# Kernel tuning notes

Hardware: AMD Instinct MI355X
Metric: run time of the kernel (lower is better)

## Reference

```python
import jax, jax.numpy as jnp
import numpy as np

N_NODES = 16  # superpixels per sample (gcn1 nodes)


def setup_inputs() -> dict:
    key = jax.random.key(0)
    ks = jax.random.split(key, 10)
    B, Cin, H, W = 32, 64, 112, 112
    Cout, H2, W2 = 128, 56, 56
    E = 64
    inp = {
        "B_for": jax.random.normal(ks[0], (B, Cin, H, W), jnp.float32),
        "B_fon": jax.random.normal(ks[1], (B, Cout, H2, W2), jnp.float32),
        "seg": jax.random.randint(ks[2], (B, H, W), 0, N_NODES, jnp.int32),
        "src": jax.random.randint(ks[3], (B, E), 0, N_NODES, jnp.int32),
        "dst": jax.random.randint(ks[4], (B, E), 0, N_NODES, jnp.int32),
        "conv_w": jax.random.normal(ks[5], (1, Cin), jnp.float32) * 0.1,
        "conv_b": jnp.zeros((1,), jnp.float32),
        "W1": jax.random.normal(ks[6], (4, 32), jnp.float32) * 0.3,
        "b1": jnp.zeros((32,), jnp.float32),
        "W2": jax.random.normal(ks[7], (32, Cout), jnp.float32) * 0.15,
        "b2": jnp.zeros((Cout,), jnp.float32),
        "fc_w": jax.random.normal(ks[8], (1, N_NODES), jnp.float32) * 0.2,
        "fc_b": jnp.zeros((1,), jnp.float32),
    }
    return inp


def _superpixel_features(L, seg):
    # L: [B,1,H,W] intensity; seg: [B,H,W] labels in [0, N_NODES)
    B, _, H, W = L.shape
    ids = (seg + jnp.arange(B, dtype=seg.dtype)[:, None, None] * N_NODES).reshape(-1)
    Lf = L[:, 0].reshape(-1)
    ones = jnp.ones_like(Lf)
    rows = jnp.broadcast_to(jnp.arange(H, dtype=L.dtype)[None, :, None], (B, H, W)).reshape(-1)
    cols = jnp.broadcast_to(jnp.arange(W, dtype=L.dtype)[None, None, :], (B, H, W)).reshape(-1)
    nseg = B * N_NODES
    cnt = jax.ops.segment_sum(ones, ids, num_segments=nseg)
    s_r = jax.ops.segment_sum(rows, ids, num_segments=nseg)
    s_c = jax.ops.segment_sum(cols, ids, num_segments=nseg)
    s_i = jax.ops.segment_sum(Lf, ids, num_segments=nseg)
    cnt_safe = jnp.maximum(cnt, 1.0)
    feats = jnp.stack([s_r / cnt_safe, s_c / cnt_safe, s_i / cnt_safe, cnt], axis=-1)
    feats = feats.reshape(B, N_NODES, 4)
    # normalize mean_intensity and area columns: (x - mean) / (std + 1), unbiased std
    sub = feats[..., 2:]
    mu = sub.mean(axis=1, keepdims=True)
    sd = jnp.std(sub, axis=1, keepdims=True, ddof=1)
    return jnp.concatenate([feats[..., :2], (sub - mu) / (sd + 1.0)], axis=-1)


def _graph_conv(A, nrm, X, Wt, bt):
    # DGL GraphConv, norm='both': D^{-1/2} A D^{-1/2} X W + b
    agg = jnp.einsum('bij,bjf->bif', A, nrm[..., None] * X)
    return nrm[..., None] * agg @ Wt + bt


def reference(B_for, B_fon, seg, src, dst, conv_w, conv_b, W1, b1, W2, b2, fc_w, fc_b):
    B = B_for.shape[0]
    # 1x1 conv -> single-channel intensity map L
    L = jnp.einsum('bchw,oc->bohw', B_for, conv_w) + conv_b[None, :, None, None]
    X = _superpixel_features(L, seg)  # [B, N, 4]
    # symmetric adjacency from edge list
    bidx = jnp.arange(B)[:, None]
    A = jnp.zeros((B, N_NODES, N_NODES), B_for.dtype)
    A = A.at[bidx, src, dst].set(1.0)
    A = A.at[bidx, dst, src].set(1.0)
    nrm = jnp.clip(A.sum(-1), 1.0, None) ** -0.5
    h1 = jax.nn.relu(_graph_conv(A, nrm, X, W1, b1))   # [B, N, 32]
    h2 = jax.nn.relu(_graph_conv(A, nrm, h1, W2, b2))  # [B, N, 128]
    # fc over nodes: Linear(N -> 1) applied to h2.T  => [B, 128]
    G = jnp.einsum('bnf,n->bf', h2, fc_w[0]) + fc_b[0]
    # broadcast-modulate dense CNN features
    return G[:, :, None, None] * B_fon
```

## Files before the change

### kernel.cpp

```cpp
#include <hip/hip_runtime.h>

#define NN 16
constexpr int BB = 32, CIN = 64, HH = 112, WW = 112;
constexpr int HWC = HH * WW;
constexpr int COUT = 128, HW2 = 56 * 56;
constexpr int NE = 64;
constexpr int NQ = HWC / 4;
constexpr int BPI = 13;
constexpr int PF4 = COUT * HW2 / 4;
constexpr int SBPB = 25;

__global__ __launch_bounds__(256) void k_conv_seg(
    const float* __restrict__ Bfor, const int* __restrict__ seg,
    const float* __restrict__ convw, float* __restrict__ part)
{
    __shared__ float w[CIN];
    __shared__ float acc[8 * 80];
    const int tid = threadIdx.x;
    const int b   = blockIdx.x / BPI;
    const int blk = blockIdx.x % BPI;

    if (tid < CIN) w[tid] = convw[tid];
    for (int i = tid; i < 8 * 80; i += 256) acc[i] = 0.f;
    __syncthreads();

    const int q = blk * 256 + tid;
    if (q < NQ) {
        const int p = q * 4;
        const float* base = Bfor + (size_t)b * CIN * HWC + p;

        float4 s = make_float4(0.f, 0.f, 0.f, 0.f);
        #pragma unroll
        for (int cb = 0; cb < 4; ++cb) {
            float4 v[16];
            #pragma unroll
            for (int j = 0; j < 16; ++j)
                v[j] = *reinterpret_cast<const float4*>(base + (size_t)(cb * 16 + j) * HWC);
            #pragma unroll
            for (int j = 0; j < 16; ++j) {
                const float wc = w[cb * 16 + j];
                s.x = fmaf(v[j].x, wc, s.x);
                s.y = fmaf(v[j].y, wc, s.y);
                s.z = fmaf(v[j].z, wc, s.z);
                s.w = fmaf(v[j].w, wc, s.w);
            }
        }

        const int4 sg = *reinterpret_cast<const int4*>(seg + (size_t)b * HWC + p);
        const float row  = (float)(p / WW);
        const float col0 = (float)(p % WW);
        const int k = tid & 7;
        float* a0 = &acc[k * 80];
        atomicAdd(a0 + sg.x * 5 + 0, row);
        atomicAdd(a0 + sg.x * 5 + 1, col0);
        atomicAdd(a0 + sg.x * 5 + 2, s.x);
        atomicAdd(a0 + sg.x * 5 + 3, 1.f);
        atomicAdd(a0 + sg.y * 5 + 0, row);
        atomicAdd(a0 + sg.y * 5 + 1, col0 + 1.f);
        atomicAdd(a0 + sg.y * 5 + 2, s.y);
        atomicAdd(a0 + sg.y * 5 + 3, 1.f);
        atomicAdd(a0 + sg.z * 5 + 0, row);
        atomicAdd(a0 + sg.z * 5 + 1, col0 + 2.f);
        atomicAdd(a0 + sg.z * 5 + 2, s.z);
        atomicAdd(a0 + sg.z * 5 + 3, 1.f);
        atomicAdd(a0 + sg.w * 5 + 0, row);
        atomicAdd(a0 + sg.w * 5 + 1, col0 + 3.f);
        atomicAdd(a0 + sg.w * 5 + 2, s.w);
        atomicAdd(a0 + sg.w * 5 + 3, 1.f);
    }
    __syncthreads();

    if (tid < NN * 4) {
        const int node = tid >> 2, st = tid & 3;
        float v = 0.f;
        #pragma unroll
        for (int k = 0; k < 8; ++k) v += acc[k * 80 + node * 5 + st];
        part[((b * BPI + blk) * NN + node) * 4 + st] = v;
    }
}

__global__ __launch_bounds__(256) void k_graph_scale(
    const float* __restrict__ part, const int* __restrict__ src,
    const int* __restrict__ dst,  const float* __restrict__ convb,
    const float* __restrict__ W1, const float* __restrict__ b1,
    const float* __restrict__ W2, const float* __restrict__ b2,
    const float* __restrict__ fcw, const float* __restrict__ fcb,
    const float* __restrict__ Bfon, float* __restrict__ out)
{
    const int b    = blockIdx.x / SBPB;
    const int blkb = blockIdx.x % SBPB;
    const int tid  = threadIdx.x;

    __shared__ float X[NN][4];
    __shared__ float A[NN][NN];
    __shared__ float nrm[NN];
    __shared__ float h1s[NN][32];
    __shared__ float agg[NN][32];
    __shared__ float gpart[2][COUT];
    __shared__ float Gs[COUT];

    if (tid < 64) {
        const int node = tid >> 2, st = tid & 3;
        float v = 0.f;
        #pragma unroll
        for (int k = 0; k < BPI; ++k) v += part[((b * BPI + k) * NN + node) * 4 + st];
        X[node][st] = v;
    }
    for (int i = tid; i < NN * NN; i += 256) ((float*)A)[i] = 0.f;
    __syncthreads();

    if (tid < NN) {
        const float cnt = X[tid][3];
        const float cs  = fmaxf(cnt, 1.f);
        X[tid][0] = X[tid][0] / cs;
        X[tid][1] = X[tid][1] / cs;
        X[tid][2] = (X[tid][2] + cnt * convb[0]) / cs;
    }
    __syncthreads();

    if (tid < 2) {
        const int c = 2 + tid;
        float mu = 0.f;
        for (int i = 0; i < NN; ++i) mu += X[i][c];
        mu *= (1.f / NN);
        float var = 0.f;
        for (int i = 0; i < NN; ++i) { const float d = X[i][c] - mu; var = fmaf(d, d, var); }
        var *= (1.f / (NN - 1));
        const float inv = 1.f / (sqrtf(var) + 1.f);
        for (int i = 0; i < NN; ++i) X[i][c] = (X[i][c] - mu) * inv;
    }
    if (tid >= 64 && tid < 64 + NE) {
        const int e = tid - 64;
        const int s = src[b * NE + e], d = dst[b * NE + e];
        A[s][d] = 1.f;
        A[d][s] = 1.f;
    }
    __syncthreads();

    if (tid < NN) {
        float rs = 0.f;
        for (int j = 0; j < NN; ++j) rs += A[tid][j];
        nrm[tid] = 1.f / sqrtf(fmaxf(rs, 1.f));
    }
    __syncthreads();

    if (tid < NN * 4) {
        const int i = tid >> 2, k = tid & 3;
        float s = 0.f;
        for (int j = 0; j < NN; ++j) s = fmaf(A[i][j] * nrm[j], X[j][k], s);
        agg[i][k] = s;
    }
    __syncthreads();

    for (int t = tid; t < NN * 32; t += 256) {
        const int i = t >> 5, f = t & 31;
        float s = 0.f;
        #pragma unroll
        for (int k = 0; k < 4; ++k) s = fmaf(agg[i][k], W1[k * 32 + f], s);
        h1s[i][f] = fmaxf(fmaf(nrm[i], s, b1[f]), 0.f);
    }
    __syncthreads();

    for (int t = tid; t < NN * 32; t += 256) {
        const int i = t >> 5, k = t & 31;
        float s = 0.f;
        for (int j = 0; j < NN; ++j) s = fmaf(A[i][j] * nrm[j], h1s[j][k], s);
        agg[i][k] = s;
    }
    __syncthreads();

    {
        const int f = tid & 127, half = tid >> 7;
        float g = 0.f;
        const float bf = b2[f];
        for (int i = half * 8; i < half * 8 + 8; ++i) {
            float s = 0.f;
            #pragma unroll
            for (int k = 0; k < 32; ++k) s = fmaf(agg[i][k], W2[k * COUT + f], s);
            g = fmaf(fcw[i], fmaxf(fmaf(nrm[i], s, bf), 0.f), g);
        }
        gpart[half][f] = g;
    }
    __syncthreads();
    if (tid < COUT) Gs[tid] = gpart[0][tid] + gpart[1][tid] + fcb[0];
    __syncthreads();

    const float4* bf4 = reinterpret_cast<const float4*>(Bfon) + (size_t)b * PF4;
    float4*       ob4 = reinterpret_cast<float4*>(out)        + (size_t)b * PF4;
    for (int t = blkb * 256 + tid; t < PF4; t += SBPB * 256) {
        const float4 v = bf4[t];
        const float  g = Gs[t / (HW2 / 4)];
        ob4[t] = make_float4(v.x * g, v.y * g, v.z * g, v.w * g);
    }
}

extern "C" void kernel_launch(void* const* d_in, const int* in_sizes, int n_in,
                              void* d_out, int out_size, void* d_ws, size_t ws_size,
                              hipStream_t stream)
{
    const float* Bfor  = (const float*)d_in[0];
    const float* Bfon  = (const float*)d_in[1];
    const int*   seg   = (const int*)d_in[2];
    const int*   src   = (const int*)d_in[3];
    const int*   dst   = (const int*)d_in[4];
    const float* convw = (const float*)d_in[5];
    const float* convb = (const float*)d_in[6];
    const float* W1    = (const float*)d_in[7];
    const float* b1    = (const float*)d_in[8];
    const float* W2    = (const float*)d_in[9];
    const float* b2    = (const float*)d_in[10];
    const float* fcw   = (const float*)d_in[11];
    const float* fcb   = (const float*)d_in[12];

    float* part = (float*)d_ws;
    float* out  = (float*)d_out;

    k_conv_seg<<<BB * BPI, 256, 0, stream>>>(Bfor, seg, convw, part);
    k_graph_scale<<<BB * SBPB, 256, 0, stream>>>(part, src, dst, convb,
                                                 W1, b1, W2, b2, fcw, fcb,
                                                 Bfon, out);
}
```

Baseline: 51.40 us.

## Split conv-seg work by channel group and image half per block

The first kernel now gives each block 8 input channels over half an image instead of all 64 channels over a 1024-pixel strip. Each thread keeps partial sums for 6-7 float4 pixel groups, and the row, column and count statistics are spread across channel groups 0-2. The graph kernel then sums 16 partials per sample. The aim is more independent loads in flight per block, at the cost of more seg reads and more shared-memory atomics for the intensity term (each channel group scatters its own partial).

```diff
diff --git a/kernel.cpp b/kernel.cpp
--- a/kernel.cpp
+++ b/kernel.cpp
@@ -6,76 +6,93 @@
 constexpr int COUT = 128, HW2 = 56 * 56;
 constexpr int NE = 64;
 constexpr int NQ = HWC / 4;
-constexpr int BPI = 13;
+constexpr int HQ = NQ / 2;
+constexpr int CPB = 8;
 constexpr int PF4 = COUT * HW2 / 4;
 constexpr int SBPB = 25;
 
-__global__ __launch_bounds__(256) void k_conv_seg(
+__global__ __launch_bounds__(256, 2) void k_conv_seg(
     const float* __restrict__ Bfor, const int* __restrict__ seg,
     const float* __restrict__ convw, float* __restrict__ part)
 {
-    __shared__ float w[CIN];
-    __shared__ float acc[8 * 80];
+    __shared__ float acc8[8 * 80];
     const int tid = threadIdx.x;
-    const int b   = blockIdx.x / BPI;
-    const int blk = blockIdx.x % BPI;
-
-    if (tid < CIN) w[tid] = convw[tid];
-    for (int i = tid; i < 8 * 80; i += 256) acc[i] = 0.f;
-    __syncthreads();
-
-    const int q = blk * 256 + tid;
-    if (q < NQ) {
-        const int p = q * 4;
-        const float* base = Bfor + (size_t)b * CIN * HWC + p;
-
-        float4 s = make_float4(0.f, 0.f, 0.f, 0.f);
-        #pragma unroll
-        for (int cb = 0; cb < 4; ++cb) {
-            float4 v[16];
-            #pragma unroll
-            for (int j = 0; j < 16; ++j)
-                v[j] = *reinterpret_cast<const float4*>(base + (size_t)(cb * 16 + j) * HWC);
-            #pragma unroll
-            for (int j = 0; j < 16; ++j) {
-                const float wc = w[cb * 16 + j];
-                s.x = fmaf(v[j].x, wc, s.x);
-                s.y = fmaf(v[j].y, wc, s.y);
-                s.z = fmaf(v[j].z, wc, s.z);
-                s.w = fmaf(v[j].w, wc, s.w);
-            }
-        }
-
-        const int4 sg = *reinterpret_cast<const int4*>(seg + (size_t)b * HWC + p);
-        const float row  = (float)(p / WW);
-        const float col0 = (float)(p % WW);
-        const int k = tid & 7;
-        float* a0 = &acc[k * 80];
-        atomicAdd(a0 + sg.x * 5 + 0, row);
-        atomicAdd(a0 + sg.x * 5 + 1, col0);
-        atomicAdd(a0 + sg.x * 5 + 2, s.x);
-        atomicAdd(a0 + sg.x * 5 + 3, 1.f);
-        atomicAdd(a0 + sg.y * 5 + 0, row);
-        atomicAdd(a0 + sg.y * 5 + 1, col0 + 1.f);
-        atomicAdd(a0 + sg.y * 5 + 2, s.y);
-        atomicAdd(a0 + sg.y * 5 + 3, 1.f);
-        atomicAdd(a0 + sg.z * 5 + 0, row);
-        atomicAdd(a0 + sg.z * 5 + 1, col0 + 2.f);
-        atomicAdd(a0 + sg.z * 5 + 2, s.z);
-        atomicAdd(a0 + sg.z * 5 + 3, 1.f);
-        atomicAdd(a0 + sg.w * 5 + 0, row);
-        atomicAdd(a0 + sg.w * 5 + 1, col0 + 3.f);
-        atomicAdd(a0 + sg.w * 5 + 2, s.w);
-        atomicAdd(a0 + sg.w * 5 + 3, 1.f);
-    }
-    __syncthreads();
-
-    if (tid < NN * 4) {
+    const int bid = blockIdx.x;
+    const int b   = bid >> 4;
+    const int h   = (bid >> 3) & 1;
+    const int cg  = bid & 7;
+
+    for (int i = tid; i < 8 * 80; i += 256) acc8[i] = 0.f;
+    __syncthreads();
+
+    float4 a[7];
+    #pragma unroll
+    for (int k = 0; k < 7; ++k) a[k] = make_float4(0.f, 0.f, 0.f, 0.f);
+
+    const float* bbase = Bfor + (size_t)(b * CIN + cg * CPB) * HWC + (size_t)h * HQ * 4;
+    #pragma unroll
+    for (int c = 0; c < CPB; ++c) {
+        const float wc = convw[cg * CPB + c];
+        const float* pl = bbase + (size_t)c * HWC + tid * 4;
+        float4 v[7];
+        #pragma unroll
+        for (int k = 0; k < 6; ++k)
+            v[k] = *reinterpret_cast<const float4*>(pl + k * 1024);
+        if (tid < 32) v[6] = *reinterpret_cast<const float4*>(pl + 6 * 1024);
+        #pragma unroll
+        for (int k = 0; k < 6; ++k) {
+            a[k].x = fmaf(v[k].x, wc, a[k].x);
+            a[k].y = fmaf(v[k].y, wc, a[k].y);
+            a[k].z = fmaf(v[k].z, wc, a[k].z);
+            a[k].w = fmaf(v[k].w, wc, a[k].w);
+        }
+        if (tid < 32) {
+            a[6].x = fmaf(v[6].x, wc, a[6].x);
+            a[6].y = fmaf(v[6].y, wc, a[6].y);
+            a[6].z = fmaf(v[6].z, wc, a[6].z);
+            a[6].w = fmaf(v[6].w, wc, a[6].w);
+        }
+    }
+
+    const int* segb = seg + (size_t)b * HWC + (size_t)h * HQ * 4;
+    const int rep = tid & 7;
+    float* ar = &acc8[rep * 80];
+    const int nk = (tid < 32) ? 7 : 6;
+    for (int k = 0; k < nk; ++k) {
+        const int q = tid + k * 256;
+        const int p = h * HQ * 4 + q * 4;
+        const int4 sg = *reinterpret_cast<const int4*>(segb + q * 4);
+        atomicAdd(ar + sg.x * 5 + 2, a[k].x);
+        atomicAdd(ar + sg.y * 5 + 2, a[k].y);
+        atomicAdd(ar + sg.z * 5 + 2, a[k].z);
+        atomicAdd(ar + sg.w * 5 + 2, a[k].w);
+        if (cg == 0) {
+            const float row = (float)(p / WW);
+            atomicAdd(ar + sg.x * 5 + 0, row);
+            atomicAdd(ar + sg.y * 5 + 0, row);
+            atomicAdd(ar + sg.z * 5 + 0, row);
+            atomicAdd(ar + sg.w * 5 + 0, row);
+        } else if (cg == 1) {
+            const float col0 = (float)(p % WW);
+            atomicAdd(ar + sg.x * 5 + 1, col0);
+            atomicAdd(ar + sg.y * 5 + 1, col0 + 1.f);
+            atomicAdd(ar + sg.z * 5 + 1, col0 + 2.f);
+            atomicAdd(ar + sg.w * 5 + 1, col0 + 3.f);
+        } else if (cg == 2) {
+            atomicAdd(ar + sg.x * 5 + 3, 1.f);
+            atomicAdd(ar + sg.y * 5 + 3, 1.f);
+            atomicAdd(ar + sg.z * 5 + 3, 1.f);
+            atomicAdd(ar + sg.w * 5 + 3, 1.f);
+        }
+    }
+    __syncthreads();
+
+    if (tid < 64) {
         const int node = tid >> 2, st = tid & 3;
         float v = 0.f;
         #pragma unroll
-        for (int k = 0; k < 8; ++k) v += acc[k * 80 + node * 5 + st];
-        part[((b * BPI + blk) * NN + node) * 4 + st] = v;
+        for (int r = 0; r < 8; ++r) v += acc8[r * 80 + node * 5 + st];
+        part[bid * 64 + node * 4 + st] = v;
     }
 }
 
@@ -100,11 +117,10 @@
     __shared__ float Gs[COUT];
 
     if (tid < 64) {
-        const int node = tid >> 2, st = tid & 3;
         float v = 0.f;
         #pragma unroll
-        for (int k = 0; k < BPI; ++k) v += part[((b * BPI + k) * NN + node) * 4 + st];
-        X[node][st] = v;
+        for (int j = 0; j < 16; ++j) v += part[(b * 16 + j) * 64 + tid];
+        X[tid >> 2][tid & 3] = v;
     }
     for (int i = tid; i < NN * NN; i += 256) ((float*)A)[i] = 0.f;
     __syncthreads();
@@ -215,7 +231,7 @@
     float* part = (float*)d_ws;
     float* out  = (float*)d_out;
 
-    k_conv_seg<<<BB * BPI, 256, 0, stream>>>(Bfor, seg, convw, part);
+    k_conv_seg<<<BB * 16, 256, 0, stream>>>(Bfor, seg, convw, part);
     k_graph_scale<<<BB * SBPB, 256, 0, stream>>>(part, src, dst, convb,
                                                  W1, b1, W2, b2, fcw, fcb,
                                                  Bfon, out);
```

Result: slower. 83.48 us (+62.4%).
